# Optimization experiments

Measured on AMD Instinct MI355X. Metric: run time of the kernel, lower is better.

The kernel has to match this reference:

```python
import jax, jax.numpy as jnp
import numpy as np

N_SPLIT = 100
MAXLEAF = 64
EMBSIZE = 32
N_TREES = 2000  # n_split * max_ntree_per_split
M_PER_SPLIT = N_TREES // N_SPLIT  # 20
BATCH = 4096


def setup_inputs() -> dict:
    key = jax.random.key(0)
    k1, k2 = jax.random.split(key)
    leaves = jax.random.randint(k1, (BATCH, N_TREES), 0, MAXLEAF, dtype=jnp.int32)
    # glorot_normal-like init for embed_w [n_split, m*maxleaf, embsize]
    fan_in, fan_out = M_PER_SPLIT * MAXLEAF, EMBSIZE
    std = (2.0 / (fan_in + fan_out)) ** 0.5
    embed_w = jax.random.normal(k2, (N_SPLIT, M_PER_SPLIT * MAXLEAF, EMBSIZE), dtype=jnp.float32) * std
    return {"leaves": leaves, "embed_w": embed_w}


def reference(leaves, embed_w):
    # Original: one_hot(leaves, maxleaf) reshaped to [B, n_split, m*maxleaf],
    # then bmm with embed_w [n_split, m*maxleaf, E].
    # Equivalent: per (batch, split), sum over the m trees of the embedding row
    # at index t*maxleaf + leaf_id. Implemented as a direct gather + sum.
    B = leaves.shape[0]
    n_split, rows, E = embed_w.shape
    m = rows // MAXLEAF
    lv = leaves.reshape(B, n_split, m).astype(jnp.int32)
    row_idx = lv + (jnp.arange(m, dtype=jnp.int32) * MAXLEAF)  # [B, n_split, m]
    split_idx = jnp.arange(n_split, dtype=jnp.int32)[None, :, None]  # [1, n_split, 1]
    gathered = embed_w[split_idx, row_idx]  # [B, n_split, m, E]
    leaf_emb = gathered.sum(axis=2)  # [B, n_split, E]
    return leaf_emb.reshape(B, n_split * E)
```

## Files before the change

### kernel.cpp

```cpp
#include <hip/hip_runtime.h>

#define NSPLIT  100
#define MTREE   20
#define MAXLEAF 64
#define EMB     32
#define NTREES  2000
#define BATCH   4096
#define OUTW    (NSPLIT*EMB)
#define SPLIT_B 81920

#define THREADS 1024
#define CHUNKS  8
#define BPC     (BATCH/CHUNKS)
#define NBLK    (NSPLIT*CHUNKS)

__device__ __forceinline__ unsigned int pk_bf16(float a, float b) {
    unsigned int r;
    asm("v_cvt_pk_bf16_f32 %0, %1, %2" : "=v"(r) : "v"(a), "v"(b));
    return r;
}

__device__ __forceinline__ void d2(float& a, unsigned int w, unsigned int sel) {
    asm("v_dot2_f32_bf16 %0, %1, %2, %0" : "+v"(a) : "v"(w), "v"(sel));
}

__global__ __launch_bounds__(THREADS, 1) void leaf2emb_v20(
    const int* __restrict__ leaves,
    const float* __restrict__ embed,
    float* __restrict__ out)
{
    __shared__ char tl[SPLIT_B];

    const int bid = blockIdx.x;
    const int wkr = (bid & 7) * (NBLK / 8) + (bid >> 3);
    const int s     = wkr >> 3;
    const int chunk = wkr & 7;

    const int tid = threadIdx.x;
    const int l   = tid & 3;
    const int g   = tid >> 2;

    {
        const float4* emb4 = (const float4*)embed + (size_t)s * 10240;
#pragma unroll 2
        for (int k = 0; k < 10; ++k) {
            const int i = tid + k * 1024;
            const float4 v = emb4[i];
            *(uint2*)(tl + i * 8) =
                make_uint2(pk_bf16(v.x, v.y), pk_bf16(v.z, v.w));
        }
    }

    const int bA = chunk * BPC + g;
    const int bB = bA + 256;
    const int4* lvA = (const int4*)(leaves + (size_t)bA * NTREES + s * MTREE);
    const int4* lvB = (const int4*)(leaves + (size_t)bB * NTREES + s * MTREE);

    int4 L0 = lvA[0], L1 = lvA[1], L2 = lvA[2], L3 = lvA[3], L4 = lvA[4];

    __syncthreads();

    const char* tb  = tl + l * 16;
    const char* tbH = tb + 65536;

    const unsigned int selL = 0x00003F80u;
    const unsigned int selH = 0x3F800000u;

#define ROWL(T, LEAF) (*(const uint4*)(tb  + (T) * 4096 + ((LEAF) << 6)))
#define ROWH(T, LEAF) (*(const uint4*)(tbH + ((T) - 16) * 4096 + ((LEAF) << 6)))
#define D2ACC(V) { \
        d2(a0.x, (V).x, selL); d2(a0.y, (V).x, selH); \
        d2(a0.z, (V).y, selL); d2(a0.w, (V).y, selH); \
        d2(a1.x, (V).z, selL); d2(a1.y, (V).z, selH); \
        d2(a1.z, (V).w, selL); d2(a1.w, (V).w, selH); }

    float4 a0 = {0,0,0,0}, a1 = {0,0,0,0};

    uint4 v00 = ROWL(0,  L0.x), v01 = ROWL(1,  L0.y), v02 = ROWL(2,  L0.z), v03 = ROWL(3,  L0.w);
    uint4 v04 = ROWL(4,  L1.x), v05 = ROWL(5,  L1.y), v06 = ROWL(6,  L1.z), v07 = ROWL(7,  L1.w);
    uint4 v08 = ROWL(8,  L2.x), v09 = ROWL(9,  L2.y), v10 = ROWL(10, L2.z), v11 = ROWL(11, L2.w);
    uint4 v12 = ROWL(12, L3.x), v13 = ROWL(13, L3.y), v14 = ROWL(14, L3.z), v15 = ROWL(15, L3.w);
    uint4 v16 = ROWH(16, L4.x), v17 = ROWH(17, L4.y), v18 = ROWH(18, L4.z), v19 = ROWH(19, L4.w);
    int4 M0 = lvB[0], M1 = lvB[1], M2 = lvB[2], M3 = lvB[3], M4 = lvB[4];
    D2ACC(v00) D2ACC(v01) D2ACC(v02) D2ACC(v03)
    D2ACC(v04) D2ACC(v05) D2ACC(v06) D2ACC(v07)
    D2ACC(v08) D2ACC(v09) D2ACC(v10) D2ACC(v11)
    D2ACC(v12) D2ACC(v13) D2ACC(v14) D2ACC(v15)
    D2ACC(v16) D2ACC(v17) D2ACC(v18) D2ACC(v19)
    {
        float* oA = out + (size_t)bA * OUTW + s * EMB + l * 8;
        *(float4*)(oA)     = a0;
        *(float4*)(oA + 4) = a1;
    }

    a0 = make_float4(0, 0, 0, 0);
    a1 = make_float4(0, 0, 0, 0);
    v00 = ROWL(0,  M0.x); v01 = ROWL(1,  M0.y); v02 = ROWL(2,  M0.z); v03 = ROWL(3,  M0.w);
    v04 = ROWL(4,  M1.x); v05 = ROWL(5,  M1.y); v06 = ROWL(6,  M1.z); v07 = ROWL(7,  M1.w);
    v08 = ROWL(8,  M2.x); v09 = ROWL(9,  M2.y); v10 = ROWL(10, M2.z); v11 = ROWL(11, M2.w);
    v12 = ROWL(12, M3.x); v13 = ROWL(13, M3.y); v14 = ROWL(14, M3.z); v15 = ROWL(15, M3.w);
    v16 = ROWH(16, M4.x); v17 = ROWH(17, M4.y); v18 = ROWH(18, M4.z); v19 = ROWH(19, M4.w);
    D2ACC(v00) D2ACC(v01) D2ACC(v02) D2ACC(v03)
    D2ACC(v04) D2ACC(v05) D2ACC(v06) D2ACC(v07)
    D2ACC(v08) D2ACC(v09) D2ACC(v10) D2ACC(v11)
    D2ACC(v12) D2ACC(v13) D2ACC(v14) D2ACC(v15)
    D2ACC(v16) D2ACC(v17) D2ACC(v18) D2ACC(v19)
    {
        float* oB = out + (size_t)bB * OUTW + s * EMB + l * 8;
        *(float4*)(oB)     = a0;
        *(float4*)(oB + 4) = a1;
    }

#undef ROWL
#undef ROWH
#undef D2ACC
}

extern "C" void kernel_launch(void* const* d_in, const int* in_sizes, int n_in,
                              void* d_out, int out_size, void* d_ws, size_t ws_size,
                              hipStream_t stream) {
    const int* leaves  = (const int*)d_in[0];
    const float* embed = (const float*)d_in[1];
    float* out         = (float*)d_out;

    leaf2emb_v20<<<dim3(NBLK), dim3(THREADS), 0, stream>>>(leaves, embed, out);
}
```

Measured before the change: 29.90 us.

## Distribute flattened (split,batch) work evenly across 512 persistent-style blocks

Replaces the fixed 800-block grid (one block per split and batch chunk) with 512 blocks that each process an equal contiguous range of the flattened split×batch space, crossing split boundaries when needed. Each block reloads and converts the split's embedding table to bf16 in LDS whenever it enters a new split, with barriers between. This aims to match the block count to the CU count and avoid a partial second wave. In exchange, some blocks stage two tables, the gather loop has dynamic bounds, and the prefetch of the second leaf row before compute is lost.

```diff
diff --git a/kernel.cpp b/kernel.cpp
--- a/kernel.cpp
+++ b/kernel.cpp
@@ -10,9 +10,8 @@
 #define SPLIT_B 81920
 
 #define THREADS 1024
-#define CHUNKS  8
-#define BPC     (BATCH/CHUNKS)
-#define NBLK    (NSPLIT*CHUNKS)
+#define NBLK    512
+#define IPB     ((BATCH*NSPLIT)/NBLK)
 
 __device__ __forceinline__ unsigned int pk_bf16(float a, float b) {
     unsigned int r;
@@ -24,7 +23,7 @@
     asm("v_dot2_f32_bf16 %0, %1, %2, %0" : "+v"(a) : "v"(w), "v"(sel));
 }
 
-__global__ __launch_bounds__(THREADS, 1) void leaf2emb_v20(
+__global__ __launch_bounds__(THREADS, 1) void leaf2emb_v23(
     const int* __restrict__ leaves,
     const float* __restrict__ embed,
     float* __restrict__ out)
@@ -33,38 +32,19 @@
 
     const int bid = blockIdx.x;
     const int wkr = (bid & 7) * (NBLK / 8) + (bid >> 3);
-    const int s     = wkr >> 3;
-    const int chunk = wkr & 7;
 
     const int tid = threadIdx.x;
     const int l   = tid & 3;
     const int g   = tid >> 2;
 
-    {
-        const float4* emb4 = (const float4*)embed + (size_t)s * 10240;
-#pragma unroll 2
-        for (int k = 0; k < 10; ++k) {
-            const int i = tid + k * 1024;
-            const float4 v = emb4[i];
-            *(uint2*)(tl + i * 8) =
-                make_uint2(pk_bf16(v.x, v.y), pk_bf16(v.z, v.w));
-        }
-    }
-
-    const int bA = chunk * BPC + g;
-    const int bB = bA + 256;
-    const int4* lvA = (const int4*)(leaves + (size_t)bA * NTREES + s * MTREE);
-    const int4* lvB = (const int4*)(leaves + (size_t)bB * NTREES + s * MTREE);
-
-    int4 L0 = lvA[0], L1 = lvA[1], L2 = lvA[2], L3 = lvA[3], L4 = lvA[4];
-
-    __syncthreads();
-
-    const char* tb  = tl + l * 16;
-    const char* tbH = tb + 65536;
+    int s      = (wkr * IPB) >> 12;
+    int bstart = (wkr * IPB) & 4095;
+    int remain = IPB;
 
     const unsigned int selL = 0x00003F80u;
     const unsigned int selH = 0x3F800000u;
+    const char* tb  = tl + l * 16;
+    const char* tbH = tb + 65536;
 
 #define ROWL(T, LEAF) (*(const uint4*)(tb  + (T) * 4096 + ((LEAF) << 6)))
 #define ROWH(T, LEAF) (*(const uint4*)(tbH + ((T) - 16) * 4096 + ((LEAF) << 6)))
@@ -74,41 +54,47 @@
         d2(a1.x, (V).z, selL); d2(a1.y, (V).z, selH); \
         d2(a1.z, (V).w, selL); d2(a1.w, (V).w, selH); }
 
-    float4 a0 = {0,0,0,0}, a1 = {0,0,0,0};
+    while (remain > 0) {
+        const int cnt = min(remain, BATCH - bstart);
 
-    uint4 v00 = ROWL(0,  L0.x), v01 = ROWL(1,  L0.y), v02 = ROWL(2,  L0.z), v03 = ROWL(3,  L0.w);
-    uint4 v04 = ROWL(4,  L1.x), v05 = ROWL(5,  L1.y), v06 = ROWL(6,  L1.z), v07 = ROWL(7,  L1.w);
-    uint4 v08 = ROWL(8,  L2.x), v09 = ROWL(9,  L2.y), v10 = ROWL(10, L2.z), v11 = ROWL(11, L2.w);
-    uint4 v12 = ROWL(12, L3.x), v13 = ROWL(13, L3.y), v14 = ROWL(14, L3.z), v15 = ROWL(15, L3.w);
-    uint4 v16 = ROWH(16, L4.x), v17 = ROWH(17, L4.y), v18 = ROWH(18, L4.z), v19 = ROWH(19, L4.w);
-    int4 M0 = lvB[0], M1 = lvB[1], M2 = lvB[2], M3 = lvB[3], M4 = lvB[4];
-    D2ACC(v00) D2ACC(v01) D2ACC(v02) D2ACC(v03)
-    D2ACC(v04) D2ACC(v05) D2ACC(v06) D2ACC(v07)
-    D2ACC(v08) D2ACC(v09) D2ACC(v10) D2ACC(v11)
-    D2ACC(v12) D2ACC(v13) D2ACC(v14) D2ACC(v15)
-    D2ACC(v16) D2ACC(v17) D2ACC(v18) D2ACC(v19)
-    {
-        float* oA = out + (size_t)bA * OUTW + s * EMB + l * 8;
-        *(float4*)(oA)     = a0;
-        *(float4*)(oA + 4) = a1;
-    }
+        if (remain != IPB) __syncthreads();
 
-    a0 = make_float4(0, 0, 0, 0);
-    a1 = make_float4(0, 0, 0, 0);
-    v00 = ROWL(0,  M0.x); v01 = ROWL(1,  M0.y); v02 = ROWL(2,  M0.z); v03 = ROWL(3,  M0.w);
-    v04 = ROWL(4,  M1.x); v05 = ROWL(5,  M1.y); v06 = ROWL(6,  M1.z); v07 = ROWL(7,  M1.w);
-    v08 = ROWL(8,  M2.x); v09 = ROWL(9,  M2.y); v10 = ROWL(10, M2.z); v11 = ROWL(11, M2.w);
-    v12 = ROWL(12, M3.x); v13 = ROWL(13, M3.y); v14 = ROWL(14, M3.z); v15 = ROWL(15, M3.w);
-    v16 = ROWH(16, M4.x); v17 = ROWH(17, M4.y); v18 = ROWH(18, M4.z); v19 = ROWH(19, M4.w);
-    D2ACC(v00) D2ACC(v01) D2ACC(v02) D2ACC(v03)
-    D2ACC(v04) D2ACC(v05) D2ACC(v06) D2ACC(v07)
-    D2ACC(v08) D2ACC(v09) D2ACC(v10) D2ACC(v11)
-    D2ACC(v12) D2ACC(v13) D2ACC(v14) D2ACC(v15)
-    D2ACC(v16) D2ACC(v17) D2ACC(v18) D2ACC(v19)
-    {
-        float* oB = out + (size_t)bB * OUTW + s * EMB + l * 8;
-        *(float4*)(oB)     = a0;
-        *(float4*)(oB + 4) = a1;
+        {
+            const float4* emb4 = (const float4*)embed + (size_t)s * 10240;
+#pragma unroll 2
+            for (int k = 0; k < 10; ++k) {
+                const int i = tid + k * 1024;
+                const float4 v = emb4[i];
+                *(uint2*)(tl + i * 8) =
+                    make_uint2(pk_bf16(v.x, v.y), pk_bf16(v.z, v.w));
+            }
+        }
+        __syncthreads();
+
+        for (int b = bstart + g; b < bstart + cnt; b += 256) {
+            const int4* lv = (const int4*)(leaves + (size_t)b * NTREES + s * MTREE);
+            const int4 L0 = lv[0], L1 = lv[1], L2 = lv[2], L3 = lv[3], L4 = lv[4];
+
+            float4 a0 = {0,0,0,0}, a1 = {0,0,0,0};
+            uint4 v00 = ROWL(0,  L0.x), v01 = ROWL(1,  L0.y), v02 = ROWL(2,  L0.z), v03 = ROWL(3,  L0.w);
+            uint4 v04 = ROWL(4,  L1.x), v05 = ROWL(5,  L1.y), v06 = ROWL(6,  L1.z), v07 = ROWL(7,  L1.w);
+            uint4 v08 = ROWL(8,  L2.x), v09 = ROWL(9,  L2.y), v10 = ROWL(10, L2.z), v11 = ROWL(11, L2.w);
+            uint4 v12 = ROWL(12, L3.x), v13 = ROWL(13, L3.y), v14 = ROWL(14, L3.z), v15 = ROWL(15, L3.w);
+            uint4 v16 = ROWH(16, L4.x), v17 = ROWH(17, L4.y), v18 = ROWH(18, L4.z), v19 = ROWH(19, L4.w);
+            D2ACC(v00) D2ACC(v01) D2ACC(v02) D2ACC(v03)
+            D2ACC(v04) D2ACC(v05) D2ACC(v06) D2ACC(v07)
+            D2ACC(v08) D2ACC(v09) D2ACC(v10) D2ACC(v11)
+            D2ACC(v12) D2ACC(v13) D2ACC(v14) D2ACC(v15)
+            D2ACC(v16) D2ACC(v17) D2ACC(v18) D2ACC(v19)
+
+            float* o_ = out + (size_t)b * OUTW + s * EMB + l * 8;
+            *(float4*)(o_)     = a0;
+            *(float4*)(o_ + 4) = a1;
+        }
+
+        remain -= cnt;
+        bstart = 0;
+        s += 1;
     }
 
 #undef ROWL
@@ -123,5 +109,5 @@
     const float* embed = (const float*)d_in[1];
     float* out         = (float*)d_out;
 
-    leaf2emb_v20<<<dim3(NBLK), dim3(THREADS), 0, stream>>>(leaves, embed, out);
+    leaf2emb_v23<<<dim3(NBLK), dim3(THREADS), 0, stream>>>(leaves, embed, out);
 }
```

After: 27.39 us. 8.4% less time.
